# Optimization experiments

Hardware: AMD Instinct MI355X
Metric: run time of the kernel (lower is better)

## Reference

```python
import jax, jax.numpy as jnp
import numpy as np

# heavy-atom counts minus 1 (the residue_len) for the 20 standard amino acids
# GLY ALA SER CYS THR VAL PRO LEU ILE ASN ASP MET GLN GLU LYS HIS PHE ARG TYR TRP
NATOMS = np.array([4,5,6,6,7,7,7,8,8,8,8,8,9,9,9,10,11,11,12,14], dtype=np.int64)
NTYPES = 20
MAXA = int(NATOMS.max())  # 14
B, R, VDIM, NLIN = 128, 512, 256, 3


def setup_inputs() -> dict:
    rng = np.random.default_rng(0)
    type_ids = rng.integers(0, NTYPES, size=R)                     # metadata.seq as type ids
    natoms = NATOMS[type_ids]                                      # per-residue atom count
    residue_indices = np.concatenate([[0], np.cumsum(natoms)[:-1]])  # start atom of each residue
    n_atoms = int(natoms.sum())

    key = jax.random.key(0)
    k1, k2, k3 = jax.random.split(key, 3)
    x = jax.random.normal(k1, (B, n_atoms, 3), dtype=jnp.float32)

    # per-type first-layer weight, zero-padded beyond each type's natom so the
    # padded gathered atoms contribute exactly zero (identical math to slicing)
    pad_mask = (np.arange(MAXA)[None, :] < NATOMS[:, None]).astype(np.float32)  # (T, A)
    W0 = jax.random.normal(k2, (NTYPES, VDIM, MAXA), dtype=jnp.float32)
    W0 = W0 * (1.0 / np.sqrt(MAXA)) * jnp.asarray(pad_mask)[:, None, :]
    Wh = jax.random.normal(k3, (NTYPES, NLIN - 1, VDIM, VDIM), dtype=jnp.float32) * (1.0 / np.sqrt(VDIM))

    return {
        "x": x,
        "W0": W0,
        "Wh": Wh,
        "type_ids": jnp.asarray(type_ids, dtype=jnp.int64),
        "residue_indices": jnp.asarray(residue_indices, dtype=jnp.int64),
    }


def reference(x, W0, Wh, type_ids, residue_indices):
    """x:(B, atoms, 3) -> pos_ca:(B, R, 3), x_v:(B, R, VDIM, 3)"""
    n_atoms = x.shape[1]
    # gather each residue's atom window, padded to MAXA (clip keeps indices in
    # range; padded entries are killed by the zero-padded W0 columns)
    atom_idx = jnp.clip(residue_indices[:, None] + jnp.arange(MAXA)[None, :], 0, n_atoms - 1)  # (R, A)
    gathered = x[:, atom_idx]                               # (B, R, A, 3)
    root = x[:, residue_indices + 1]                        # (B, R, 3)  -- CA atom (x[:,1] of each slice)
    delta = gathered - root[:, :, None, :]                  # subtract root

    h = jnp.einsum('rva,brac->brvc', W0[type_ids], delta)   # per-type VecLinear(natom -> vdim)
    for l in range(NLIN - 1):                               # per-type VecLinear(vdim -> vdim)
        h = jnp.einsum('rvu,bruc->brvc', Wh[type_ids, l], h)

    pos_ca = root                                            # x[:, residue_indices + 1]
    return pos_ca, h
```

## Files before the change

### kernel.cpp

```cpp
#include <hip/hip_runtime.h>

namespace {
constexpr int NB = 128;
constexpr int NR = 512;
constexpr int ND = 256;
constexpr int NA = 14;

using short8 = __attribute__((ext_vector_type(8))) short;
using f32x4  = __attribute__((ext_vector_type(4))) float;

constexpr size_t WH_US  = (size_t)40 * 16 * 8 * 64 * 8;
constexpr size_t W0_OFF = WH_US;
constexpr size_t W0_US  = (size_t)20 * 16 * 64 * 8;
constexpr size_t RMAP_BYTE_OFF = (WH_US + W0_US) * 2;
constexpr size_t WS_NEEDED = RMAP_BYTE_OFF + NR * sizeof(int);

__device__ __forceinline__ unsigned short f2bf(float f) {
    unsigned int u = __float_as_uint(f);
    u = (u + 0x7FFFu + ((u >> 16) & 1u)) >> 16;
    return (unsigned short)u;
}
}

__global__ void conv_wh(const float* __restrict__ Wh, unsigned short* __restrict__ ws) {
    int g = blockIdx.x * 256 + threadIdx.x;
    if (g >= 40 * 16 * 8 * 64) return;
    const int lane = g & 63, kt = (g >> 6) & 7, mt = (g >> 9) & 15, tl = g >> 13;
    const int v = mt * 16 + (lane & 15);
    const int u0 = kt * 32 + (lane >> 4) * 8;
    const float* src = Wh + ((size_t)tl * ND + v) * ND + u0;
    unsigned short o[8];
#pragma unroll
    for (int j = 0; j < 8; ++j) o[j] = f2bf(src[j]);
    uint4 pk;
    pk.x = o[0] | ((unsigned)o[1] << 16); pk.y = o[2] | ((unsigned)o[3] << 16);
    pk.z = o[4] | ((unsigned)o[5] << 16); pk.w = o[6] | ((unsigned)o[7] << 16);
    *reinterpret_cast<uint4*>(ws + (size_t)g * 8) = pk;
}

__global__ void conv_w0(const float* __restrict__ W0, unsigned short* __restrict__ ws) {
    int g = blockIdx.x * 256 + threadIdx.x;
    if (g >= 20 * 16 * 64) return;
    const int lane = g & 63, mt = (g >> 6) & 15, t = g >> 10;
    const int v = mt * 16 + (lane & 15);
    const int a0 = (lane >> 4) * 8;
    unsigned short o[8];
#pragma unroll
    for (int j = 0; j < 8; ++j) {
        const int a = a0 + j;
        o[j] = (a < NA) ? f2bf(W0[((size_t)t * ND + v) * NA + a]) : (unsigned short)0;
    }
    uint4 pk;
    pk.x = o[0] | ((unsigned)o[1] << 16); pk.y = o[2] | ((unsigned)o[3] << 16);
    pk.z = o[4] | ((unsigned)o[5] << 16); pk.w = o[6] | ((unsigned)o[7] << 16);
    *reinterpret_cast<uint4*>(ws + W0_OFF + (size_t)g * 8) = pk;
}

__global__ void build_rmap(const int* __restrict__ type_ids, int* __restrict__ rmap) {
    __shared__ int tl[NR];
    const int tid = threadIdx.x;
    tl[tid] = type_ids[tid];
    __syncthreads();
    const int myt = tl[tid];
    int pos = 0;
    for (int j = 0; j < NR; ++j) {
        const int tj = tl[j];
        pos += (tj < myt) || (tj == myt && j < tid);
    }
    rmap[pos] = tid;
}

__global__ __launch_bounds__(512, 4) void residues_mfma(
    const float* __restrict__ x, const unsigned short* __restrict__ wsw,
    const int* __restrict__ rmap, const int* __restrict__ type_ids,
    const int* __restrict__ res_idx, float* __restrict__ out, int n_atoms)
{
    const int tid = threadIdx.x, lane = tid & 63, w = tid >> 6;
    const int xcd = blockIdx.x & 7, j = blockIdx.x >> 3;
    const int r = rmap[xcd * 64 + (j >> 2)];
    const int b0 = (j & 3) * 32;
    const int ri = res_idx[r], t = type_ids[r];

    __shared__ __align__(16) unsigned short HT[96 * 264];
    unsigned short* dltT = HT;

    const unsigned short* w0b = wsw + W0_OFF + (size_t)t * (16 * 64 * 8);
    short8 a0[2];
#pragma unroll
    for (int mi = 0; mi < 2; ++mi)
        a0[mi] = *reinterpret_cast<const short8*>(w0b + (((w * 2 + mi) * 64) + lane) * 8);

#pragma unroll
    for (int it = 0; it < 2; ++it) {
        const int task = tid + it * 512;
        const int bl = task >> 5, k = task & 31;
        const float* xb = x + (size_t)(b0 + bl) * n_atoms * 3;
        if (k < 16) {
            int atom = ri + k; if (atom > n_atoms - 1) atom = n_atoms - 1;
            const float* src  = xb + (size_t)atom * 3;
            const float* root = xb + (size_t)(ri + 1) * 3;
#pragma unroll
            for (int c = 0; c < 3; ++c)
                dltT[(bl * 3 + c) * 40 + k] = f2bf(src[c] - root[c]);
            if (k == 1) {
#pragma unroll
                for (int c = 0; c < 3; ++c)
                    out[((size_t)(b0 + bl) * NR + r) * 3 + c] = root[c];
            }
        } else {
#pragma unroll
            for (int c = 0; c < 3; ++c)
                dltT[(bl * 3 + c) * 40 + k] = 0;
        }
    }
    __syncthreads();

    f32x4 acc[2][6];
#pragma unroll
    for (int mi = 0; mi < 2; ++mi)
#pragma unroll
        for (int ni = 0; ni < 6; ++ni) acc[mi][ni] = f32x4{0.f, 0.f, 0.f, 0.f};

    {
        short8 bf[6];
#pragma unroll
        for (int ni = 0; ni < 6; ++ni)
            bf[ni] = *reinterpret_cast<const short8*>(&dltT[(ni * 16 + (lane & 15)) * 40 + (lane >> 4) * 8]);
#pragma unroll
        for (int mi = 0; mi < 2; ++mi)
#pragma unroll
            for (int ni = 0; ni < 6; ++ni)
                acc[mi][ni] = __builtin_amdgcn_mfma_f32_16x16x32_bf16(a0[mi], bf[ni], acc[mi][ni], 0, 0, 0);
    }
    __syncthreads();

#pragma unroll 1
    for (int l = 0; l < 2; ++l) {
#pragma unroll
        for (int mi = 0; mi < 2; ++mi)
#pragma unroll
            for (int ni = 0; ni < 6; ++ni) {
                const int v0 = w * 32 + mi * 16 + (lane >> 4) * 4;
                const int n  = ni * 16 + (lane & 15);
                const unsigned lo = (unsigned)f2bf(acc[mi][ni][0]) | ((unsigned)f2bf(acc[mi][ni][1]) << 16);
                const unsigned hi = (unsigned)f2bf(acc[mi][ni][2]) | ((unsigned)f2bf(acc[mi][ni][3]) << 16);
                *reinterpret_cast<uint2*>(&HT[n * 264 + v0]) = make_uint2(lo, hi);
            }
        __syncthreads();

#pragma unroll
        for (int mi = 0; mi < 2; ++mi)
#pragma unroll
            for (int ni = 0; ni < 6; ++ni) acc[mi][ni] = f32x4{0.f, 0.f, 0.f, 0.f};

        const unsigned short* wl = wsw + (size_t)(t * 2 + l) * (16 * 8 * 64 * 8);
        short8 a_cur[2], a_nxt[2];
#pragma unroll
        for (int mi = 0; mi < 2; ++mi)
            a_cur[mi] = *reinterpret_cast<const short8*>(wl + ((((w * 2 + mi) * 8) * 64) + lane) * 8);
#pragma unroll 1
        for (int kt = 0; kt < 8; ++kt) {
            if (kt < 7) {
#pragma unroll
                for (int mi = 0; mi < 2; ++mi)
                    a_nxt[mi] = *reinterpret_cast<const short8*>(wl + ((((w * 2 + mi) * 8 + kt + 1) * 64) + lane) * 8);
            }
            short8 bf[6];
#pragma unroll
            for (int ni = 0; ni < 6; ++ni)
                bf[ni] = *reinterpret_cast<const short8*>(&HT[(ni * 16 + (lane & 15)) * 264 + kt * 32 + (lane >> 4) * 8]);
#pragma unroll
            for (int mi = 0; mi < 2; ++mi)
#pragma unroll
                for (int ni = 0; ni < 6; ++ni)
                    acc[mi][ni] = __builtin_amdgcn_mfma_f32_16x16x32_bf16(a_cur[mi], bf[ni], acc[mi][ni], 0, 0, 0);
#pragma unroll
            for (int mi = 0; mi < 2; ++mi) a_cur[mi] = a_nxt[mi];
        }
        if (l == 0) __syncthreads();
    }

    float* fst  = reinterpret_cast<float*>(HT);
    float* outh = out + (size_t)NB * NR * 3;
#pragma unroll 1
    for (int p = 0; p < 2; ++p) {
        __syncthreads();
        if ((w >> 2) == p) {
            const int wq = w & 3;
#pragma unroll
            for (int mi = 0; mi < 2; ++mi)
#pragma unroll
                for (int ni = 0; ni < 6; ++ni) {
                    const int n = ni * 16 + (lane & 15);
#pragma unroll
                    for (int jj = 0; jj < 4; ++jj) {
                        const int vl = wq * 32 + mi * 16 + (lane >> 4) * 4 + jj;
                        fst[n * 132 + vl] = acc[mi][ni][jj];
                    }
                }
        }
        __syncthreads();
#pragma unroll
        for (int i = 0; i < 6; ++i) {
            const int idx = tid + i * 512;
            const int bl = idx / 96, g = idx % 96;
            f32x4 v4;
#pragma unroll
            for (int e = 0; e < 4; ++e) {
                const int f = 4 * g + e, c = f % 3, vp = f / 3;
                v4[e] = fst[(bl * 3 + c) * 132 + vp];
            }
            __builtin_nontemporal_store(v4,
                reinterpret_cast<f32x4*>(&outh[(((size_t)(b0 + bl) * NR + r) * (ND * 3)) + p * 384 + 4 * g]));
        }
    }
}

__global__ __launch_bounds__(256, 3) void residues_fused_fb(
    const float* __restrict__ x, const float* __restrict__ W0,
    const float* __restrict__ Wh, const int* __restrict__ type_ids,
    const int* __restrict__ res_idx, float* __restrict__ out, int n_atoms)
{
    const int tid = threadIdx.x;
    const int r = blockIdx.x >> 4;
    const int b0 = (blockIdx.x & 15) * 8;
    const int ri = res_idx[r], t = type_ids[r];
    __shared__ float dlt[NA][24];
    __shared__ float hA[ND][24];
    __shared__ float hB[ND][24];
    for (int idx = tid; idx < 8 * NA * 3; idx += 256) {
        const int bb = idx / (NA * 3), rem = idx % (NA * 3);
        const int a = rem / 3, c = rem % 3, b = b0 + bb;
        int ca = ri + a; if (ca > n_atoms - 1) ca = n_atoms - 1;
        const float root = x[((size_t)b * n_atoms + (ri + 1)) * 3 + c];
        dlt[a][bb * 3 + c] = x[((size_t)b * n_atoms + ca) * 3 + c] - root;
        if (a == 0) out[((size_t)b * NR + r) * 3 + c] = root;
    }
    __syncthreads();
    {
        const float* w0row = W0 + ((size_t)t * ND + tid) * NA;
        float acc[24];
#pragma unroll
        for (int n = 0; n < 24; ++n) acc[n] = 0.f;
#pragma unroll
        for (int a = 0; a < NA; ++a) {
            const float wv = w0row[a];
#pragma unroll
            for (int n = 0; n < 24; ++n) acc[n] += wv * dlt[a][n];
        }
#pragma unroll
        for (int n = 0; n < 24; ++n) hA[tid][n] = acc[n];
    }
    __syncthreads();
    const float* whbase = Wh + (size_t)t * 2 * ND * ND;
#pragma unroll
    for (int l = 0; l < 2; ++l) {
        const float* wrow = whbase + ((size_t)l * ND + tid) * ND;
        const float (*hin)[24] = (l == 0) ? hA : hB;
        float (*hout)[24]      = (l == 0) ? hB : hA;
        float acc[24];
#pragma unroll
        for (int n = 0; n < 24; ++n) acc[n] = 0.f;
        for (int u = 0; u < ND; ++u) {
            const float wv = wrow[u];
#pragma unroll
            for (int n = 0; n < 24; ++n) acc[n] += wv * hin[u][n];
        }
#pragma unroll
        for (int n = 0; n < 24; ++n) hout[tid][n] = acc[n];
        __syncthreads();
    }
    float* outh = out + (size_t)NB * NR * 3;
#pragma unroll
    for (int bb = 0; bb < 8; ++bb) {
        const size_t base = ((size_t)((b0 + bb) * NR + r)) * (ND * 3);
#pragma unroll
        for (int it = 0; it < 3; ++it) {
            const int g = it * 256 + tid;
            outh[base + g] = hA[g / 3][bb * 3 + g % 3];
        }
    }
}

extern "C" void kernel_launch(void* const* d_in, const int* in_sizes, int n_in,
                              void* d_out, int out_size, void* d_ws, size_t ws_size,
                              hipStream_t stream) {
    const float* x        = (const float*)d_in[0];
    const float* W0       = (const float*)d_in[1];
    const float* Wh       = (const float*)d_in[2];
    const int*   type_ids = (const int*)d_in[3];
    const int*   res_idx  = (const int*)d_in[4];
    float* out = (float*)d_out;
    const int n_atoms = in_sizes[0] / (NB * 3);

    if (ws_size >= WS_NEEDED) {
        unsigned short* wsw = (unsigned short*)d_ws;
        int* rmap = (int*)((char*)d_ws + RMAP_BYTE_OFF);
        conv_wh<<<(40 * 16 * 8 * 64 + 255) / 256, 256, 0, stream>>>(Wh, wsw);
        conv_w0<<<(20 * 16 * 64 + 255) / 256, 256, 0, stream>>>(W0, wsw);
        build_rmap<<<1, NR, 0, stream>>>(type_ids, rmap);
        residues_mfma<<<NR * 4, 512, 0, stream>>>(x, wsw, rmap, type_ids, res_idx, out, n_atoms);
    } else {
        residues_fused_fb<<<NR * 16, 256, 0, stream>>>(x, W0, Wh, type_ids, res_idx, out, n_atoms);
    }
}
```

Before: 97.82 us.

## Merge weight-conversion and rmap prep kernels, cut registers to raise occupancy

Folds the three preprocessing kernels (Wh conversion, W0 conversion, residue sort map) into one launch split by block index, removing two kernel launches. In the main MFMA kernel it drops the A-operand register prefetch and the six-wide B-fragment register array, loading operands just before use. The launch bound rises from 4 to 6 waves-per-SIMD minimum so more blocks can be resident to hide latency. The cost is less software prefetching of global weight loads, and the rmap block now runs a serial loop over two residues per thread.

```diff
diff --git a/kernel.cpp b/kernel.cpp
--- a/kernel.cpp
+++ b/kernel.cpp
@@ -22,55 +22,58 @@
 }
 }
 
-__global__ void conv_wh(const float* __restrict__ Wh, unsigned short* __restrict__ ws) {
-    int g = blockIdx.x * 256 + threadIdx.x;
-    if (g >= 40 * 16 * 8 * 64) return;
-    const int lane = g & 63, kt = (g >> 6) & 7, mt = (g >> 9) & 15, tl = g >> 13;
-    const int v = mt * 16 + (lane & 15);
-    const int u0 = kt * 32 + (lane >> 4) * 8;
-    const float* src = Wh + ((size_t)tl * ND + v) * ND + u0;
-    unsigned short o[8];
-#pragma unroll
-    for (int j = 0; j < 8; ++j) o[j] = f2bf(src[j]);
-    uint4 pk;
-    pk.x = o[0] | ((unsigned)o[1] << 16); pk.y = o[2] | ((unsigned)o[3] << 16);
-    pk.z = o[4] | ((unsigned)o[5] << 16); pk.w = o[6] | ((unsigned)o[7] << 16);
-    *reinterpret_cast<uint4*>(ws + (size_t)g * 8) = pk;
-}
-
-__global__ void conv_w0(const float* __restrict__ W0, unsigned short* __restrict__ ws) {
-    int g = blockIdx.x * 256 + threadIdx.x;
-    if (g >= 20 * 16 * 64) return;
-    const int lane = g & 63, mt = (g >> 6) & 15, t = g >> 10;
-    const int v = mt * 16 + (lane & 15);
-    const int a0 = (lane >> 4) * 8;
-    unsigned short o[8];
-#pragma unroll
-    for (int j = 0; j < 8; ++j) {
-        const int a = a0 + j;
-        o[j] = (a < NA) ? f2bf(W0[((size_t)t * ND + v) * NA + a]) : (unsigned short)0;
-    }
-    uint4 pk;
-    pk.x = o[0] | ((unsigned)o[1] << 16); pk.y = o[2] | ((unsigned)o[3] << 16);
-    pk.z = o[4] | ((unsigned)o[5] << 16); pk.w = o[6] | ((unsigned)o[7] << 16);
-    *reinterpret_cast<uint4*>(ws + W0_OFF + (size_t)g * 8) = pk;
-}
-
-__global__ void build_rmap(const int* __restrict__ type_ids, int* __restrict__ rmap) {
+__global__ __launch_bounds__(256) void prep_all(
+    const float* __restrict__ Wh, const float* __restrict__ W0,
+    const int* __restrict__ type_ids,
+    unsigned short* __restrict__ ws, int* __restrict__ rmap)
+{
     __shared__ int tl[NR];
-    const int tid = threadIdx.x;
-    tl[tid] = type_ids[tid];
-    __syncthreads();
-    const int myt = tl[tid];
-    int pos = 0;
-    for (int j = 0; j < NR; ++j) {
-        const int tj = tl[j];
-        pos += (tj < myt) || (tj == myt && j < tid);
-    }
-    rmap[pos] = tid;
-}
-
-__global__ __launch_bounds__(512, 4) void residues_mfma(
+    const int bid = blockIdx.x, tid = threadIdx.x;
+    if (bid < 1280) {
+        const int g = bid * 256 + tid;
+        const int lane = g & 63, kt = (g >> 6) & 7, mt = (g >> 9) & 15, tw = g >> 13;
+        const int v = mt * 16 + (lane & 15);
+        const int u0 = kt * 32 + (lane >> 4) * 8;
+        const float* src = Wh + ((size_t)tw * ND + v) * ND + u0;
+        unsigned short o[8];
+#pragma unroll
+        for (int j = 0; j < 8; ++j) o[j] = f2bf(src[j]);
+        uint4 pk;
+        pk.x = o[0] | ((unsigned)o[1] << 16); pk.y = o[2] | ((unsigned)o[3] << 16);
+        pk.z = o[4] | ((unsigned)o[5] << 16); pk.w = o[6] | ((unsigned)o[7] << 16);
+        *reinterpret_cast<uint4*>(ws + (size_t)g * 8) = pk;
+    } else if (bid < 1360) {
+        const int g = (bid - 1280) * 256 + tid;
+        const int lane = g & 63, mt = (g >> 6) & 15, t = g >> 10;
+        const int v = mt * 16 + (lane & 15);
+        const int a0 = (lane >> 4) * 8;
+        unsigned short o[8];
+#pragma unroll
+        for (int j = 0; j < 8; ++j) {
+            const int a = a0 + j;
+            o[j] = (a < NA) ? f2bf(W0[((size_t)t * ND + v) * NA + a]) : (unsigned short)0;
+        }
+        uint4 pk;
+        pk.x = o[0] | ((unsigned)o[1] << 16); pk.y = o[2] | ((unsigned)o[3] << 16);
+        pk.z = o[4] | ((unsigned)o[5] << 16); pk.w = o[6] | ((unsigned)o[7] << 16);
+        *reinterpret_cast<uint4*>(ws + W0_OFF + (size_t)g * 8) = pk;
+    } else {
+        tl[tid] = type_ids[tid];
+        tl[tid + 256] = type_ids[tid + 256];
+        __syncthreads();
+        for (int i = tid; i < NR; i += 256) {
+            const int myt = tl[i];
+            int pos = 0;
+            for (int j = 0; j < NR; ++j) {
+                const int tj = tl[j];
+                pos += (tj < myt) || (tj == myt && j < i);
+            }
+            rmap[pos] = i;
+        }
+    }
+}
+
+__global__ __launch_bounds__(512, 6) void residues_mfma(
     const float* __restrict__ x, const unsigned short* __restrict__ wsw,
     const int* __restrict__ rmap, const int* __restrict__ type_ids,
     const int* __restrict__ res_idx, float* __restrict__ out, int n_atoms)
@@ -121,16 +124,12 @@
 #pragma unroll
         for (int ni = 0; ni < 6; ++ni) acc[mi][ni] = f32x4{0.f, 0.f, 0.f, 0.f};
 
-    {
-        short8 bf[6];
-#pragma unroll
-        for (int ni = 0; ni < 6; ++ni)
-            bf[ni] = *reinterpret_cast<const short8*>(&dltT[(ni * 16 + (lane & 15)) * 40 + (lane >> 4) * 8]);
+#pragma unroll
+    for (int ni = 0; ni < 6; ++ni) {
+        const short8 bf = *reinterpret_cast<const short8*>(&dltT[(ni * 16 + (lane & 15)) * 40 + (lane >> 4) * 8]);
 #pragma unroll
         for (int mi = 0; mi < 2; ++mi)
-#pragma unroll
-            for (int ni = 0; ni < 6; ++ni)
-                acc[mi][ni] = __builtin_amdgcn_mfma_f32_16x16x32_bf16(a0[mi], bf[ni], acc[mi][ni], 0, 0, 0);
+            acc[mi][ni] = __builtin_amdgcn_mfma_f32_16x16x32_bf16(a0[mi], bf, acc[mi][ni], 0, 0, 0);
     }
     __syncthreads();
 
@@ -154,28 +153,19 @@
             for (int ni = 0; ni < 6; ++ni) acc[mi][ni] = f32x4{0.f, 0.f, 0.f, 0.f};
 
         const unsigned short* wl = wsw + (size_t)(t * 2 + l) * (16 * 8 * 64 * 8);
-        short8 a_cur[2], a_nxt[2];
-#pragma unroll
-        for (int mi = 0; mi < 2; ++mi)
-            a_cur[mi] = *reinterpret_cast<const short8*>(wl + ((((w * 2 + mi) * 8) * 64) + lane) * 8);
 #pragma unroll 1
         for (int kt = 0; kt < 8; ++kt) {
-            if (kt < 7) {
+            short8 a[2];
+#pragma unroll
+            for (int mi = 0; mi < 2; ++mi)
+                a[mi] = *reinterpret_cast<const short8*>(wl + ((((w * 2 + mi) * 8 + kt) * 64) + lane) * 8);
+#pragma unroll
+            for (int ni = 0; ni < 6; ++ni) {
+                const short8 bf = *reinterpret_cast<const short8*>(&HT[(ni * 16 + (lane & 15)) * 264 + kt * 32 + (lane >> 4) * 8]);
 #pragma unroll
                 for (int mi = 0; mi < 2; ++mi)
-                    a_nxt[mi] = *reinterpret_cast<const short8*>(wl + ((((w * 2 + mi) * 8 + kt + 1) * 64) + lane) * 8);
-            }
-            short8 bf[6];
-#pragma unroll
-            for (int ni = 0; ni < 6; ++ni)
-                bf[ni] = *reinterpret_cast<const short8*>(&HT[(ni * 16 + (lane & 15)) * 264 + kt * 32 + (lane >> 4) * 8]);
-#pragma unroll
-            for (int mi = 0; mi < 2; ++mi)
-#pragma unroll
-                for (int ni = 0; ni < 6; ++ni)
-                    acc[mi][ni] = __builtin_amdgcn_mfma_f32_16x16x32_bf16(a_cur[mi], bf[ni], acc[mi][ni], 0, 0, 0);
-#pragma unroll
-            for (int mi = 0; mi < 2; ++mi) a_cur[mi] = a_nxt[mi];
+                    acc[mi][ni] = __builtin_amdgcn_mfma_f32_16x16x32_bf16(a[mi], bf, acc[mi][ni], 0, 0, 0);
+            }
         }
         if (l == 0) __syncthreads();
     }
@@ -296,9 +286,7 @@
     if (ws_size >= WS_NEEDED) {
         unsigned short* wsw = (unsigned short*)d_ws;
         int* rmap = (int*)((char*)d_ws + RMAP_BYTE_OFF);
-        conv_wh<<<(40 * 16 * 8 * 64 + 255) / 256, 256, 0, stream>>>(Wh, wsw);
-        conv_w0<<<(20 * 16 * 64 + 255) / 256, 256, 0, stream>>>(W0, wsw);
-        build_rmap<<<1, NR, 0, stream>>>(type_ids, rmap);
+        prep_all<<<1361, 256, 0, stream>>>(Wh, W0, type_ids, wsw, rmap);
         residues_mfma<<<NR * 4, 512, 0, stream>>>(x, wsw, rmap, type_ids, res_idx, out, n_atoms);
     } else {
         residues_fused_fb<<<NR * 16, 256, 0, stream>>>(x, W0, Wh, type_ids, res_idx, out, n_atoms);
```

Measured after the change: 131.5 us. 1.34x slower.
